# Performance work log

Hardware: AMD Instinct MI355X
Metric: run time of the kernel (lower is better)

Reference implementation:

```python
import jax, jax.numpy as jnp
import numpy as np

B, C, S, HID = 64, 512, 28, 256  # batch, channels, spatial size, LSTM hidden


def _param(k, shape):
    return jax.random.normal(k, shape, jnp.float32) * 0.05


def setup_inputs() -> dict:
    key = jax.random.key(0)
    ks = jax.random.split(key, 19)
    inp = {"x": jax.random.normal(ks[0], (B, C, S, S), jnp.float32)}
    # vertical bidirectional LSTM (input C, hidden HID), torch gate order i,f,g,o
    inp["v_wih_f"] = _param(ks[1], (4 * HID, C))
    inp["v_whh_f"] = _param(ks[2], (4 * HID, HID))
    inp["v_b_f"] = _param(ks[3], (4 * HID,))
    inp["v_wih_b"] = _param(ks[4], (4 * HID, C))
    inp["v_whh_b"] = _param(ks[5], (4 * HID, HID))
    inp["v_b_b"] = _param(ks[6], (4 * HID,))
    # horizontal bidirectional LSTM (input 2*HID=512, hidden HID)
    inp["h_wih_f"] = _param(ks[7], (4 * HID, 2 * HID))
    inp["h_whh_f"] = _param(ks[8], (4 * HID, HID))
    inp["h_b_f"] = _param(ks[9], (4 * HID,))
    inp["h_wih_b"] = _param(ks[10], (4 * HID, 2 * HID))
    inp["h_whh_b"] = _param(ks[11], (4 * HID, HID))
    inp["h_b_b"] = _param(ks[12], (4 * HID,))
    # 1x1 conv 512 -> 100 (10x10 attention kernel logits)
    inp["conv_w"] = _param(ks[13], (100, 2 * HID))
    inp["conv_b"] = _param(ks[14], (100,))
    return inp


def _lstm_scan(xs, wih, whh, b):
    # xs: [T, N, D] -> h sequence [T, N, HID]
    hdim = whh.shape[1]
    def step(carry, xt):
        h, c = carry
        gates = xt @ wih.T + h @ whh.T + b  # [N, 4H]
        i, f, g, o = jnp.split(gates, 4, axis=-1)
        c = jax.nn.sigmoid(f) * c + jax.nn.sigmoid(i) * jnp.tanh(g)
        h = jax.nn.sigmoid(o) * jnp.tanh(c)
        return (h, c), h
    n = xs.shape[1]
    z = jnp.zeros((n, hdim), xs.dtype)
    _, hs = jax.lax.scan(step, (z, z), xs)
    return hs


def _bilstm(x, wf, uf, bf, wb, ub, bb):
    # x: [N, T, D] -> [N, T, 2*HID]
    xs = jnp.swapaxes(x, 0, 1)
    hf = _lstm_scan(xs, wf, uf, bf)
    hb = _lstm_scan(xs[::-1], wb, ub, bb)[::-1]
    return jnp.swapaxes(jnp.concatenate([hf, hb], axis=-1), 0, 1)


def reference(x, v_wih_f, v_whh_f, v_b_f, v_wih_b, v_whh_b, v_b_b,
              h_wih_f, h_whh_f, h_b_f, h_wih_b, h_whh_b, h_b_b,
              conv_w, conv_b):
    b, c, s, _ = x.shape
    xt = jnp.transpose(x, (0, 3, 2, 1))            # [B, W, H, C]
    # vertical LSTM: seq over W, batched over (B, H)
    v_in = jnp.transpose(xt, (0, 2, 1, 3)).reshape(b * s, s, c)
    v_out = _bilstm(v_in, v_wih_f, v_whh_f, v_b_f, v_wih_b, v_whh_b, v_b_b)
    v_out = jnp.transpose(v_out.reshape(b, s, s, 2 * HID), (0, 2, 1, 3))  # [B, W, H, 512]
    # horizontal LSTM: seq over H, batched over (B, W)
    h_in = v_out.reshape(b * s, s, 2 * HID)
    h_out = _bilstm(h_in, h_wih_f, h_whh_f, h_b_f, h_wih_b, h_whh_b, h_b_b)
    feat = jnp.transpose(h_out.reshape(b, s, s, 2 * HID), (0, 3, 2, 1))  # [B, 512, H, W]
    # 1x1 conv -> [B, 100, H, W], softmax over 100 kernel entries
    kern = jnp.einsum('bfhw,of->bohw', feat, conv_w) + conv_b[None, :, None, None]
    kern = jax.nn.softmax(kern, axis=1)
    # faithful to torch: C-order reshape [B,100,H,W] -> (B*H*W, 100) kernels
    w = kern.reshape(b, s * s, 100)
    # grouped dilated conv3d == weighted sum over dilation-3 sampled 10x10 grid
    x_s = x[:, :, ::3, ::3].reshape(b, c, 100)     # [B, C, 100]
    out = jnp.einsum('bpk,bck->bpc', w, x_s)       # [B, H*W, C]
    return out.reshape(b, c, s, s)                 # faithful C-order reshape
```

## Files before the change

### kernel.cpp

```cpp
#include <hip/hip_runtime.h>
#include <hip/hip_bf16.h>
#include <stdint.h>

typedef __hip_bfloat16 bf16_t;
typedef __attribute__((ext_vector_type(8))) short short8;
typedef __attribute__((ext_vector_type(4))) float f32x4;
typedef __attribute__((ext_vector_type(4))) unsigned int u32x4;

#define MFMA16(a, b, c) __builtin_amdgcn_mfma_f32_16x16x32_bf16(a, b, c, 0, 0, 0)

#define NROW 50176
#define NBATCH 1792

__device__ __forceinline__ void g2l16(const void* g, void* l) {
  __builtin_amdgcn_global_load_lds(
      (const __attribute__((address_space(1))) unsigned int*)g,
      (__attribute__((address_space(3))) unsigned int*)l, 16, 0, 0);
}
__device__ __forceinline__ float sigm(float x) { return 1.0f / (1.0f + __expf(-x)); }
__device__ __forceinline__ float tanh_(float x) { return 2.0f / (1.0f + __expf(-2.0f * x)) - 1.0f; }
__device__ __forceinline__ void stc(bf16_t* p, float v) { *p = __float2bfloat16(v); }
__device__ __forceinline__ void stc(float* p, float v) { *p = v; }
__device__ __forceinline__ float bf2f(unsigned short u) {
  return __uint_as_float((unsigned int)u << 16);
}

struct CvtArgs {
  const float* src[8];
  bf16_t* dst[8];
  int n[8];
};
__global__ void cvt_all(CvtArgs a) {
  int arr = blockIdx.y;
  int i = blockIdx.x * 256 + threadIdx.x;
  if (i < a.n[arr]) a.dst[arr][i] = __float2bfloat16(a.src[arr][i]);
}

__global__ void transpose_x(const float* __restrict__ x, bf16_t* __restrict__ Xin) {
  int c0 = blockIdx.x * 128, h = blockIdx.y, b = blockIdx.z;
  __shared__ __align__(16) short tile[128 * 29];
  const float* xb = x + ((size_t)b * 512 + c0) * 784 + h * 28;
  for (int e = threadIdx.x; e < 128 * 28; e += 256) {
    int cc = e / 28, w = e - cc * 28;
    tile[cc * 29 + w] = __bfloat16_as_short(__float2bfloat16(xb[(size_t)cc * 784 + w]));
  }
  __syncthreads();
  short* outb = (short*)Xin + ((size_t)(b * 28 + h) * 28) * 512 + c0;
  for (int e = threadIdx.x; e < 28 * 128; e += 256) {
    int w = e >> 7, cc = e & 127;
    outb[(size_t)w * 512 + cc] = tile[cc * 29 + w];
  }
}

__global__ void build_xs(const float* __restrict__ x, bf16_t* __restrict__ xs) {
  int c = blockIdx.x, b = blockIdx.y;
  int k = threadIdx.x;
  const float* xr = x + ((size_t)b * 512 + c) * 784;
  float v = 0.0f;
  if (k < 100) { int kh = k / 10, kw = k - kh * 10; v = xr[kh * 84 + kw * 3]; }
  xs[((size_t)b * 512 + c) * 128 + k] = __float2bfloat16(v);
}

__global__ void pad_conv(const float* __restrict__ cw, const float* __restrict__ cb,
                         bf16_t* __restrict__ cwp, float* __restrict__ cbp,
                         unsigned int* __restrict__ bar) {
  int r = blockIdx.x;
  if (r == 0)
    for (int i = threadIdx.x; i < 1792; i += 128) bar[i] = 0;
  for (int i = threadIdx.x; i < 512; i += 128)
    cwp[r * 512 + i] = __float2bfloat16((r < 100) ? cw[r * 512 + i] : 0.0f);
  if (r == 0) cbp[threadIdx.x] = (threadIdx.x < 100) ? cb[threadIdx.x] : 0.0f;
}

template <typename CT>
__global__ __launch_bounds__(256) void gemm_bt(
    const bf16_t* __restrict__ A, const bf16_t* __restrict__ B0,
    const bf16_t* __restrict__ B1, int nsplit, const float* __restrict__ bias0,
    const float* __restrict__ bias1, CT* __restrict__ C, int M, int N, int K) {
  __shared__ __align__(16) short As[128 * 32];
  __shared__ __align__(16) short Bs[128 * 32];
  int tid = threadIdx.x;
  int bm0 = blockIdx.y * 128, bn0 = blockIdx.x * 128;
  const bf16_t* Bp;
  const float* biasp;
  if (bn0 < nsplit) { Bp = B0 + (size_t)bn0 * K; biasp = bias0 + bn0; }
  else { Bp = B1 + (size_t)(bn0 - nsplit) * K; biasp = bias1 + (bn0 - nsplit); }
  int lrow = tid >> 2, lseg = tid & 3;
  const char* Ag = (const char*)(A + (size_t)(bm0 + lrow) * K) + lseg * 16;
  const char* Bg = (const char*)(Bp + (size_t)lrow * K) + lseg * 16;
  size_t radv = (size_t)64 * K * 2;
  int w = tid >> 6, l = tid & 63, lm = l & 15, lq = l >> 4;
  int wm = w & 1, wn = w >> 1;
  f32x4 acc[4][4] = {};
  for (int k0 = 0; k0 < K; k0 += 32) {
    g2l16(Ag, (char*)As + tid * 16);
    g2l16(Ag + radv, (char*)As + 4096 + tid * 16);
    g2l16(Bg, (char*)Bs + tid * 16);
    g2l16(Bg + radv, (char*)Bs + 4096 + tid * 16);
    Ag += 64; Bg += 64;
    __syncthreads();
    short8 afr[4], bfr[4];
#pragma unroll
    for (int i = 0; i < 4; i++) {
      afr[i] = *(const short8*)&As[(wm * 64 + i * 16 + lm) * 32 + lq * 8];
      bfr[i] = *(const short8*)&Bs[(wn * 64 + i * 16 + lm) * 32 + lq * 8];
    }
#pragma unroll
    for (int mi = 0; mi < 4; mi++)
#pragma unroll
      for (int ni = 0; ni < 4; ni++) acc[mi][ni] = MFMA16(afr[mi], bfr[ni], acc[mi][ni]);
    __syncthreads();
  }
  float bv[4];
#pragma unroll
  for (int ni = 0; ni < 4; ni++) bv[ni] = biasp[wn * 64 + ni * 16 + lm];
#pragma unroll
  for (int mi = 0; mi < 4; mi++)
#pragma unroll
    for (int ni = 0; ni < 4; ni++) {
      int col = bn0 + wn * 64 + ni * 16 + lm;
#pragma unroll
      for (int r = 0; r < 4; r++) {
        size_t row = bm0 + wm * 64 + mi * 16 + lq * 4 + r;
        stc(&C[row * N + col], acc[mi][ni][r] + bv[ni]);
      }
    }
}

__global__ __launch_bounds__(256, 2) void lstm_scan(
    const bf16_t* __restrict__ G, const bf16_t* __restrict__ whh_f,
    const bf16_t* __restrict__ whh_b, bf16_t* __restrict__ hA,
    bf16_t* __restrict__ hB, bf16_t* __restrict__ outb,
    unsigned int* __restrict__ bar) {
  int dir = blockIdx.y;
  int js = blockIdx.x & 7;
  int rg = blockIdx.x >> 3;
  int tid = threadIdx.x, w = tid >> 6, l = tid & 63, lm = l & 15, lq = l >> 4;
  const short* whh = (const short*)(dir ? whh_b : whh_f);
  __shared__ __align__(16) short Ws[128 * 256];
  __shared__ __align__(16) short ht[64 * 40];
#pragma unroll
  for (int i = 0; i < 16; i++) {
    int segid = i * 256 + tid;
    int row = segid >> 5, seg = segid & 31;
    int gate = row >> 5, jj = row & 31;
    short8 v = *(const short8*)&whh[((size_t)(gate * 256 + js * 32 + jj)) * 256 + seg * 8];
    *(short8*)&Ws[row * 256 + ((seg ^ (row & 7)) * 8)] = v;
  }
  __syncthreads();
  unsigned int* cnt = bar + (dir * 28 + rg) * 16;
  int r0 = rg * 64 + w * 16;
  const unsigned short* Gb = (const unsigned short*)G + (size_t)dir * 1024 + js * 32;
  float creg[2][4] = {};
  unsigned short gvs[2][4][4];
  auto load_gvs = [&](int tt) {
#pragma unroll
    for (int nj = 0; nj < 2; nj++)
#pragma unroll
      for (int r = 0; r < 4; r++) {
        int bi = r0 + lq * 4 + r;
        const unsigned short* gp = Gb + ((size_t)bi * 28 + tt) * 2048 + nj * 16 + lm;
#pragma unroll
        for (int gate = 0; gate < 4; gate++) gvs[nj][gate][r] = gp[gate * 256];
      }
  };
  load_gvs(dir ? 27 : 0);
#pragma unroll 1
  for (int s = 0; s < 28; s++) {
    int t = dir ? 27 - s : s;
    f32x4 acc[4][2] = {};
    if (s > 0) {
      const unsigned long long* hrp =
          (const unsigned long long*)(((s & 1) ? hA : hB) + (size_t)dir * NBATCH * 256);
      unsigned long long hq[8][2];
#pragma unroll
      for (int kk = 0; kk < 8; kk++) {
        size_t base = ((size_t)(r0 + lm) * 256 + (size_t)(kk * 32 + lq * 8)) >> 2;
        hq[kk][0] = __hip_atomic_load(hrp + base, __ATOMIC_RELAXED, __HIP_MEMORY_SCOPE_AGENT);
        hq[kk][1] =
            __hip_atomic_load(hrp + base + 1, __ATOMIC_RELAXED, __HIP_MEMORY_SCOPE_AGENT);
      }
#pragma unroll
      for (int kk = 0; kk < 8; kk++) {
        short8 a;
        ((unsigned long long*)&a)[0] = hq[kk][0];
        ((unsigned long long*)&a)[1] = hq[kk][1];
        int bseg = ((kk * 4 + lq) ^ (lm & 7)) * 8;
#pragma unroll
        for (int gate = 0; gate < 4; gate++)
#pragma unroll
          for (int nj = 0; nj < 2; nj++) {
            short8 b = *(const short8*)&Ws[(gate * 32 + nj * 16 + lm) * 256 + bseg];
            acc[gate][nj] = MFMA16(a, b, acc[gate][nj]);
          }
      }
    }
#pragma unroll
    for (int nj = 0; nj < 2; nj++)
#pragma unroll
      for (int r = 0; r < 4; r++) {
        float gi = bf2f(gvs[nj][0][r]) + acc[0][nj][r];
        float gf = bf2f(gvs[nj][1][r]) + acc[1][nj][r];
        float gg = bf2f(gvs[nj][2][r]) + acc[2][nj][r];
        float go = bf2f(gvs[nj][3][r]) + acc[3][nj][r];
        float cn = sigm(gf) * creg[nj][r] + sigm(gi) * tanh_(gg);
        float hn = sigm(go) * tanh_(cn);
        creg[nj][r] = cn;
        ht[(w * 16 + lq * 4 + r) * 40 + nj * 16 + lm] =
            __bfloat16_as_short(__float2bfloat16(hn));
      }
    if (s < 27) load_gvs(dir ? 26 - s : s + 1);
    __syncthreads();
    {
      int row = tid >> 2, seg = tid & 3;
      u32x4 v = *(const u32x4*)&ht[row * 40 + seg * 8];
      int bi = rg * 64 + row;
      unsigned long long* hwp =
          (unsigned long long*)(((s & 1) ? hB : hA) + (size_t)dir * NBATCH * 256);
      size_t hb = ((size_t)bi * 256 + (size_t)(js * 32 + seg * 8)) >> 2;
      unsigned long long q0 = ((const unsigned long long*)&v)[0];
      unsigned long long q1 = ((const unsigned long long*)&v)[1];
      __hip_atomic_store(hwp + hb, q0, __ATOMIC_RELAXED, __HIP_MEMORY_SCOPE_AGENT);
      __hip_atomic_store(hwp + hb + 1, q1, __ATOMIC_RELAXED, __HIP_MEMORY_SCOPE_AGENT);
      int bb = bi / 28, rr = bi - bb * 28;
      *(u32x4*)((short*)outb + (((size_t)bb * 784) + (size_t)t * 28 + rr) * 512 +
                dir * 256 + js * 32 + seg * 8) = v;
    }
    if (s < 27) {
      asm volatile("s_waitcnt vmcnt(0)" ::: "memory");
      __syncthreads();
      if (tid == 0) {
        __hip_atomic_fetch_add(cnt, 1u, __ATOMIC_RELAXED, __HIP_MEMORY_SCOPE_AGENT);
        unsigned int tgt = 8u * (unsigned)(s + 1);
        while (__hip_atomic_load(cnt, __ATOMIC_RELAXED, __HIP_MEMORY_SCOPE_AGENT) < tgt)
          __builtin_amdgcn_s_sleep(2);
      }
      __syncthreads();
      __builtin_amdgcn_sched_barrier(0);
    }
  }
}

__global__ void softmax_scatter(const float* __restrict__ P, bf16_t* __restrict__ Wscr) {
  int row = blockIdx.x;
  int l = threadIdx.x;
  int b = row / 784, q = row - b * 784;
  const float* pr = P + (size_t)row * 128;
  float v0 = (l < 100) ? pr[l] : -1e30f;
  float v1 = (l + 64 < 100) ? pr[l + 64] : -1e30f;
  float m = fmaxf(v0, v1);
  for (int off = 32; off > 0; off >>= 1) m = fmaxf(m, __shfl_down(m, off));
  m = __shfl(m, 0);
  float e0 = (l < 100) ? __expf(v0 - m) : 0.0f;
  float e1 = (l + 64 < 100) ? __expf(v1 - m) : 0.0f;
  float sum = e0 + e1;
  for (int off = 32; off > 0; off >>= 1) sum += __shfl_down(sum, off);
  sum = __shfl(sum, 0);
  float inv = 1.0f / sum;
  size_t base = (size_t)b * 784 * 128;
  if (l < 100) {
    int mm = l * 784 + q;
    Wscr[base + (size_t)(mm / 100) * 128 + (mm % 100)] = __float2bfloat16(e0 * inv);
  }
  int o = l + 64;
  if (o < 100) {
    int mm = o * 784 + q;
    Wscr[base + (size_t)(mm / 100) * 128 + (mm % 100)] = __float2bfloat16(e1 * inv);
  }
}

__global__ __launch_bounds__(256) void final_gemm(const bf16_t* __restrict__ Wscr,
                                                  const bf16_t* __restrict__ xs,
                                                  float* __restrict__ outp) {
  int m0 = blockIdx.x * 112, n0 = blockIdx.y * 128, b = blockIdx.z;
  int tid = threadIdx.x, w = tid >> 6, l = tid & 63, lm = l & 15, lq = l >> 4;
  const short* Ab = (const short*)Wscr + (size_t)b * 784 * 128;
  const short* Bb = (const short*)xs + (size_t)b * 512 * 128;
  f32x4 acc[7][2] = {};
#pragma unroll
  for (int kk = 0; kk < 4; kk++) {
    short8 b0 = *(const short8*)&Bb[(size_t)(n0 + w * 32 + lm) * 128 + kk * 32 + lq * 8];
    short8 b1 = *(const short8*)&Bb[(size_t)(n0 + w * 32 + 16 + lm) * 128 + kk * 32 + lq * 8];
#pragma unroll
    for (int mi = 0; mi < 7; mi++) {
      short8 a = *(const short8*)&Ab[(size_t)(m0 + mi * 16 + lm) * 128 + kk * 32 + lq * 8];
      acc[mi][0] = MFMA16(a, b0, acc[mi][0]);
      acc[mi][1] = MFMA16(a, b1, acc[mi][1]);
    }
  }
#pragma unroll
  for (int mi = 0; mi < 7; mi++)
#pragma unroll
    for (int ni = 0; ni < 2; ni++) {
      int c = n0 + w * 32 + ni * 16 + lm;
#pragma unroll
      for (int r = 0; r < 4; r++) {
        int p = m0 + mi * 16 + lq * 4 + r;
        outp[(size_t)b * 401408 + (size_t)p * 512 + c] = acc[mi][ni][r];
      }
    }
}

extern "C" void kernel_launch(void* const* d_in, const int* in_sizes, int n_in,
                              void* d_out, int out_size, void* d_ws, size_t ws_size,
                              hipStream_t stream) {
  const float* x = (const float*)d_in[0];
  const float* v_wih_f = (const float*)d_in[1];
  const float* v_whh_f = (const float*)d_in[2];
  const float* v_b_f = (const float*)d_in[3];
  const float* v_wih_b = (const float*)d_in[4];
  const float* v_whh_b = (const float*)d_in[5];
  const float* v_b_b = (const float*)d_in[6];
  const float* h_wih_f = (const float*)d_in[7];
  const float* h_whh_f = (const float*)d_in[8];
  const float* h_b_f = (const float*)d_in[9];
  const float* h_wih_b = (const float*)d_in[10];
  const float* h_whh_b = (const float*)d_in[11];
  const float* h_b_b = (const float*)d_in[12];
  const float* conv_w = (const float*)d_in[13];
  const float* conv_b = (const float*)d_in[14];

  char* ws = (char*)d_ws;
  bf16_t* Xin = (bf16_t*)(ws);
  bf16_t* Vout = (bf16_t*)(ws + 51380224);
  bf16_t* G = (bf16_t*)(ws + 102760448);
  float* P = (float*)(ws + 102760448);
  bf16_t* Wscr = (bf16_t*)(ws + 128450560);
  bf16_t* xs = (bf16_t*)(ws + 308281344);
  bf16_t* cwp = (bf16_t*)(ws + 316669952);
  float* cbp = (float*)(ws + 316801024);
  bf16_t* hstate = (bf16_t*)(ws + 316801536);
  unsigned int* bar = (unsigned int*)(ws + 318636544);
  bf16_t* wvf = (bf16_t*)(ws + 322306560);
  bf16_t* wvb = (bf16_t*)(ws + 323355136);
  bf16_t* uvf = (bf16_t*)(ws + 324403712);
  bf16_t* uvb = (bf16_t*)(ws + 324928000);
  bf16_t* whf = (bf16_t*)(ws + 325452288);
  bf16_t* whb = (bf16_t*)(ws + 326500864);
  bf16_t* uhf = (bf16_t*)(ws + 327549440);
  bf16_t* uhb = (bf16_t*)(ws + 328073728);
  bf16_t* Hout = Xin;

  CvtArgs ca;
  ca.src[0] = v_wih_f; ca.dst[0] = wvf; ca.n[0] = 524288;
  ca.src[1] = v_wih_b; ca.dst[1] = wvb; ca.n[1] = 524288;
  ca.src[2] = v_whh_f; ca.dst[2] = uvf; ca.n[2] = 262144;
  ca.src[3] = v_whh_b; ca.dst[3] = uvb; ca.n[3] = 262144;
  ca.src[4] = h_wih_f; ca.dst[4] = whf; ca.n[4] = 524288;
  ca.src[5] = h_wih_b; ca.dst[5] = whb; ca.n[5] = 524288;
  ca.src[6] = h_whh_f; ca.dst[6] = uhf; ca.n[6] = 262144;
  ca.src[7] = h_whh_b; ca.dst[7] = uhb; ca.n[7] = 262144;
  cvt_all<<<dim3(2048, 8), 256, 0, stream>>>(ca);

  transpose_x<<<dim3(4, 28, 64), 256, 0, stream>>>(x, Xin);
  build_xs<<<dim3(512, 64), 128, 0, stream>>>(x, xs);
  pad_conv<<<dim3(128), 128, 0, stream>>>(conv_w, conv_b, cwp, cbp, bar);

  gemm_bt<bf16_t><<<dim3(16, 392), 256, 0, stream>>>(
      Xin, wvf, wvb, 1024, v_b_f, v_b_b, G, NROW, 2048, 512);
  lstm_scan<<<dim3(224, 2), 256, 0, stream>>>(G, uvf, uvb, hstate, Xin, Vout, bar);

  gemm_bt<bf16_t><<<dim3(16, 392), 256, 0, stream>>>(
      Vout, whf, whb, 1024, h_b_f, h_b_b, G, NROW, 2048, 512);
  lstm_scan<<<dim3(224, 2), 256, 0, stream>>>(G, uhf, uhb, hstate, Vout, Hout, bar + 896);

  gemm_bt<float><<<dim3(1, 392), 256, 0, stream>>>(
      Hout, cwp, cwp, 1024, cbp, cbp, P, NROW, 128, 512);
  softmax_scatter<<<dim3(50176), 64, 0, stream>>>(P, Wscr);
  final_gemm<<<dim3(7, 4, 64), 256, 0, stream>>>(Wscr, xs, (float*)d_out);
}
```

Baseline: 1.114 ms.

## Use channel-blocked activation layout and per-block gate permutation in GEMM and LSTM

Activations (input, LSTM outputs and hidden state) are stored in a channel-blocked layout of 32-channel slabs, so GEMM A tiles and LSTM h reads and writes become contiguous 64-byte segments. The input-projection GEMM now permutes its output columns so each LSTM block's four gates for its 32 hidden units sit in one contiguous 128-column chunk, which makes the per-step gate loads local. This trades some extra index arithmetic and a more complex weight row mapping for better coalescing in the latency-bound recurrent scan.

Result: faster. 1.044 ms (-6.3%).

```diff
diff --git a/kernel.cpp b/kernel.cpp
--- a/kernel.cpp
+++ b/kernel.cpp
@@ -45,10 +45,12 @@
     tile[cc * 29 + w] = __bfloat16_as_short(__float2bfloat16(xb[(size_t)cc * 784 + w]));
   }
   __syncthreads();
-  short* outb = (short*)Xin + ((size_t)(b * 28 + h) * 28) * 512 + c0;
+  size_t orow0 = (size_t)(b * 28 + h) * 28;
+  short* os = (short*)Xin;
   for (int e = threadIdx.x; e < 28 * 128; e += 256) {
     int w = e >> 7, cc = e & 127;
-    outb[(size_t)w * 512 + cc] = tile[cc * 29 + w];
+    int c = c0 + cc;
+    os[(size_t)(c >> 5) * NROW * 32 + (orow0 + w) * 32 + (c & 31)] = tile[cc * 29 + w];
   }
 }
 
@@ -72,32 +74,45 @@
   if (r == 0) cbp[threadIdx.x] = (threadIdx.x < 100) ? cb[threadIdx.x] : 0.0f;
 }
 
-template <typename CT>
+template <typename CT, bool CPERM>
 __global__ __launch_bounds__(256) void gemm_bt(
     const bf16_t* __restrict__ A, const bf16_t* __restrict__ B0,
-    const bf16_t* __restrict__ B1, int nsplit, const float* __restrict__ bias0,
+    const bf16_t* __restrict__ B1, const float* __restrict__ bias0,
     const float* __restrict__ bias1, CT* __restrict__ C, int M, int N, int K) {
   __shared__ __align__(16) short As[128 * 32];
   __shared__ __align__(16) short Bs[128 * 32];
   int tid = threadIdx.x;
-  int bm0 = blockIdx.y * 128, bn0 = blockIdx.x * 128;
-  const bf16_t* Bp;
+  int nb = blockIdx.x;
+  int bm0 = blockIdx.y * 128, bn0 = nb * 128;
+  int lrow = tid >> 2, lseg = tid & 3;
+  const char* Ag = (const char*)A + ((size_t)(bm0 + lrow) * 32 + lseg * 8) * 2;
+  size_t Aadv = (size_t)M * 64;
   const float* biasp;
-  if (bn0 < nsplit) { Bp = B0 + (size_t)bn0 * K; biasp = bias0 + bn0; }
-  else { Bp = B1 + (size_t)(bn0 - nsplit) * K; biasp = bias1 + (bn0 - nsplit); }
-  int lrow = tid >> 2, lseg = tid & 3;
-  const char* Ag = (const char*)(A + (size_t)(bm0 + lrow) * K) + lseg * 16;
-  const char* Bg = (const char*)(Bp + (size_t)lrow * K) + lseg * 16;
-  size_t radv = (size_t)64 * K * 2;
+  const char *Bg1, *Bg2;
+  int js = 0;
+  if (CPERM) {
+    int dir = nb >> 3;
+    js = nb & 7;
+    const bf16_t* Bsel = dir ? B1 : B0;
+    biasp = dir ? bias1 : bias0;
+    int br1 = (lrow >> 5) * 256 + js * 32 + (lrow & 31);
+    int br2 = ((lrow + 64) >> 5) * 256 + js * 32 + (lrow & 31);
+    Bg1 = (const char*)(B0 + 0, Bsel + (size_t)br1 * K) + lseg * 16;
+    Bg2 = (const char*)(Bsel + (size_t)br2 * K) + lseg * 16;
+  } else {
+    biasp = bias0 + bn0;
+    Bg1 = (const char*)(B0 + (size_t)(bn0 + lrow) * K) + lseg * 16;
+    Bg2 = Bg1 + (size_t)64 * K * 2;
+  }
   int w = tid >> 6, l = tid & 63, lm = l & 15, lq = l >> 4;
   int wm = w & 1, wn = w >> 1;
   f32x4 acc[4][4] = {};
   for (int k0 = 0; k0 < K; k0 += 32) {
     g2l16(Ag, (char*)As + tid * 16);
-    g2l16(Ag + radv, (char*)As + 4096 + tid * 16);
-    g2l16(Bg, (char*)Bs + tid * 16);
-    g2l16(Bg + radv, (char*)Bs + 4096 + tid * 16);
-    Ag += 64; Bg += 64;
+    g2l16(Ag + 4096, (char*)As + 4096 + tid * 16);
+    g2l16(Bg1, (char*)Bs + tid * 16);
+    g2l16(Bg2, (char*)Bs + 4096 + tid * 16);
+    Ag += Aadv; Bg1 += 64; Bg2 += 64;
     __syncthreads();
     short8 afr[4], bfr[4];
 #pragma unroll
@@ -113,7 +128,10 @@
   }
   float bv[4];
 #pragma unroll
-  for (int ni = 0; ni < 4; ni++) bv[ni] = biasp[wn * 64 + ni * 16 + lm];
+  for (int ni = 0; ni < 4; ni++) {
+    int cb = wn * 64 + ni * 16 + lm;
+    bv[ni] = CPERM ? biasp[(cb >> 5) * 256 + js * 32 + (cb & 31)] : biasp[cb];
+  }
 #pragma unroll
   for (int mi = 0; mi < 4; mi++)
 #pragma unroll
@@ -150,7 +168,8 @@
   __syncthreads();
   unsigned int* cnt = bar + (dir * 28 + rg) * 16;
   int r0 = rg * 64 + w * 16;
-  const unsigned short* Gb = (const unsigned short*)G + (size_t)dir * 1024 + js * 32;
+  size_t dbase = (size_t)dir * 458752;
+  const unsigned short* Gb = (const unsigned short*)G + (size_t)dir * 1024 + js * 128;
   float creg[2][4] = {};
   unsigned short gvs[2][4][4];
   auto load_gvs = [&](int tt) {
@@ -161,7 +180,7 @@
         int bi = r0 + lq * 4 + r;
         const unsigned short* gp = Gb + ((size_t)bi * 28 + tt) * 2048 + nj * 16 + lm;
 #pragma unroll
-        for (int gate = 0; gate < 4; gate++) gvs[nj][gate][r] = gp[gate * 256];
+        for (int gate = 0; gate < 4; gate++) gvs[nj][gate][r] = gp[gate * 32];
       }
   };
   load_gvs(dir ? 27 : 0);
@@ -171,14 +190,15 @@
     f32x4 acc[4][2] = {};
     if (s > 0) {
       const unsigned long long* hrp =
-          (const unsigned long long*)(((s & 1) ? hA : hB) + (size_t)dir * NBATCH * 256);
+          (const unsigned long long*)((s & 1) ? hA : hB);
       unsigned long long hq[8][2];
 #pragma unroll
       for (int kk = 0; kk < 8; kk++) {
-        size_t base = ((size_t)(r0 + lm) * 256 + (size_t)(kk * 32 + lq * 8)) >> 2;
-        hq[kk][0] = __hip_atomic_load(hrp + base, __ATOMIC_RELAXED, __HIP_MEMORY_SCOPE_AGENT);
-        hq[kk][1] =
-            __hip_atomic_load(hrp + base + 1, __ATOMIC_RELAXED, __HIP_MEMORY_SCOPE_AGENT);
+        size_t off = dbase + (size_t)kk * 57344 + (size_t)(r0 + lm) * 32 + lq * 8;
+        hq[kk][0] =
+            __hip_atomic_load(hrp + (off >> 2), __ATOMIC_RELAXED, __HIP_MEMORY_SCOPE_AGENT);
+        hq[kk][1] = __hip_atomic_load(hrp + (off >> 2) + 1, __ATOMIC_RELAXED,
+                                      __HIP_MEMORY_SCOPE_AGENT);
       }
 #pragma unroll
       for (int kk = 0; kk < 8; kk++) {
@@ -215,16 +235,16 @@
       int row = tid >> 2, seg = tid & 3;
       u32x4 v = *(const u32x4*)&ht[row * 40 + seg * 8];
       int bi = rg * 64 + row;
-      unsigned long long* hwp =
-          (unsigned long long*)(((s & 1) ? hB : hA) + (size_t)dir * NBATCH * 256);
-      size_t hb = ((size_t)bi * 256 + (size_t)(js * 32 + seg * 8)) >> 2;
+      unsigned long long* hwp = (unsigned long long*)((s & 1) ? hB : hA);
+      size_t off = dbase + (size_t)js * 57344 + (size_t)bi * 32 + seg * 8;
       unsigned long long q0 = ((const unsigned long long*)&v)[0];
       unsigned long long q1 = ((const unsigned long long*)&v)[1];
-      __hip_atomic_store(hwp + hb, q0, __ATOMIC_RELAXED, __HIP_MEMORY_SCOPE_AGENT);
-      __hip_atomic_store(hwp + hb + 1, q1, __ATOMIC_RELAXED, __HIP_MEMORY_SCOPE_AGENT);
+      __hip_atomic_store(hwp + (off >> 2), q0, __ATOMIC_RELAXED, __HIP_MEMORY_SCOPE_AGENT);
+      __hip_atomic_store(hwp + (off >> 2) + 1, q1, __ATOMIC_RELAXED,
+                         __HIP_MEMORY_SCOPE_AGENT);
       int bb = bi / 28, rr = bi - bb * 28;
-      *(u32x4*)((short*)outb + (((size_t)bb * 784) + (size_t)t * 28 + rr) * 512 +
-                dir * 256 + js * 32 + seg * 8) = v;
+      short* ob = (short*)outb + (size_t)(dir * 8 + js) * NROW * 32;
+      *(u32x4*)&ob[((size_t)bb * 784 + (size_t)t * 28 + rr) * 32 + seg * 8] = v;
     }
     if (s < 27) {
       asm volatile("s_waitcnt vmcnt(0)" ::: "memory");
@@ -356,16 +376,16 @@
   build_xs<<<dim3(512, 64), 128, 0, stream>>>(x, xs);
   pad_conv<<<dim3(128), 128, 0, stream>>>(conv_w, conv_b, cwp, cbp, bar);
 
-  gemm_bt<bf16_t><<<dim3(16, 392), 256, 0, stream>>>(
-      Xin, wvf, wvb, 1024, v_b_f, v_b_b, G, NROW, 2048, 512);
+  gemm_bt<bf16_t, true><<<dim3(16, 392), 256, 0, stream>>>(
+      Xin, wvf, wvb, v_b_f, v_b_b, G, NROW, 2048, 512);
   lstm_scan<<<dim3(224, 2), 256, 0, stream>>>(G, uvf, uvb, hstate, Xin, Vout, bar);
 
-  gemm_bt<bf16_t><<<dim3(16, 392), 256, 0, stream>>>(
-      Vout, whf, whb, 1024, h_b_f, h_b_b, G, NROW, 2048, 512);
+  gemm_bt<bf16_t, true><<<dim3(16, 392), 256, 0, stream>>>(
+      Vout, whf, whb, h_b_f, h_b_b, G, NROW, 2048, 512);
   lstm_scan<<<dim3(224, 2), 256, 0, stream>>>(G, uhf, uhb, hstate, Vout, Hout, bar + 896);
 
-  gemm_bt<float><<<dim3(1, 392), 256, 0, stream>>>(
-      Hout, cwp, cwp, 1024, cbp, cbp, P, NROW, 128, 512);
+  gemm_bt<float, false><<<dim3(1, 392), 256, 0, stream>>>(
+      Hout, cwp, cwp, cbp, cbp, P, NROW, 128, 512);
   softmax_scatter<<<dim3(50176), 64, 0, stream>>>(P, Wscr);
   final_gemm<<<dim3(7, 4, 64), 256, 0, stream>>>(Wscr, xs, (float*)d_out);
 }
```
